# Kernel optimization log

Hardware: AMD Instinct MI355X
Metric: run time of the kernel (lower is better)

The kernel has to match this reference:

```python
import jax, jax.numpy as jnp
import numpy as np
from jax import lax

B, L, D = 2, 2048, 128
H, HD = 8, 32
WIN = 3

def setup_inputs() -> dict:
    key = jax.random.key(0)
    ks = jax.random.split(key, 7)
    s = 0.05
    return {
        "x":  jax.random.normal(ks[0], (B, L, D), jnp.float32),
        "pe": jax.random.normal(ks[1], (L, D), jnp.float32) * s,
        "Wq": jax.random.normal(ks[2], (D, H * HD), jnp.float32) * s,
        "bq": jnp.zeros((H * HD,), jnp.float32),
        "Wk": jax.random.normal(ks[3], (D, H * HD), jnp.float32) * s,
        "bk": jnp.zeros((H * HD,), jnp.float32),
        "Wv": jax.random.normal(ks[4], (D, H), jnp.float32) * s,
    }

def reference(x, pe, Wq, bq, Wk, bk, Wv):
    b, l, d = x.shape
    h = Wv.shape[1]
    hd = Wq.shape[1] // h
    xp = x + pe                                   # (B,L,D)
    # split heads: Dense output columns [i*hd:(i+1)*hd] -> head i
    q = (xp @ Wq + bq).reshape(b, l, h, hd).transpose(2, 0, 1, 3)  # (H,B,L,hd)
    k = (xp @ Wk + bk).reshape(b, l, h, hd).transpose(2, 0, 1, 3)  # (H,B,L,hd)
    v = jax.nn.sigmoid(x @ Wv).transpose(2, 0, 1)                  # (H,B,L)

    attn = jnp.einsum('hbqd,hbkd->hbqk', q, k) * (float(hd) ** -0.5)
    attn = jax.nn.softmax(attn, axis=-1)          # (H,B,L,L)

    # band_part(0,-1) + diag_part(k=(0,L-1)) (RIGHT_LEFT align) + transpose + reverse(-2,-1)
    # collapses to the skew-gather: R[p, m] = attn[L-1-p-m, L-1-p] for p+m <= L-1 else 0
    p = jnp.arange(l)[:, None]                    # (L,1)
    m = jnp.arange(l)[None, :]                    # (1,L)
    ii = l - 1 - p - m                            # row index  (L,L)
    jj = jnp.broadcast_to(l - 1 - p, (l, l))      # col index  (L,L)
    valid = (ii >= 0)
    R = attn[:, :, jnp.where(valid, ii, 0), jj] * valid.astype(attn.dtype)  # (H,B,L,L)

    R = R * v[:, :, :, None]                      # gate by value, broadcast over distance axis

    # TF avg_pool excludes padding from the divisor
    sums = lax.reduce_window(R, 0.0, lax.add, (1, 1, 1, WIN), (1, 1, 1, 1), 'SAME')
    cnt = lax.reduce_window(jnp.ones((l,), R.dtype), 0.0, lax.add, (WIN,), (1,), 'SAME')
    pooled = sums / cnt                           # (H,B,L,L)

    # global mode: sum over position axis, -> (B, L_dist, H)
    out = pooled.sum(axis=2).transpose(1, 2, 0)
    return out
```

## Files before the change

kernel.cpp:

```cpp
#include <hip/hip_runtime.h>
#include <hip/hip_bf16.h>

#define LSEQ 2048
#define BB 2
#define DD 128
#define HH 8
#define HD 32

#define FPSCALE 524288.0f
#define RFPSCALE (1.0f / 524288.0f)
#define DENSCALE 65536.0f
#define QSCALE 0.25503486f

typedef __bf16 bf8_t __attribute__((ext_vector_type(8)));
typedef __bf16 bf4_t __attribute__((ext_vector_type(4)));
typedef float f4_t __attribute__((ext_vector_type(4)));

__global__ __launch_bounds__(256) void k_A(const float* __restrict__ x,
                                           const float* __restrict__ pe,
                                           const float* __restrict__ Wq,
                                           const float* __restrict__ Wk,
                                           const float* __restrict__ Wv,
                                           const float* __restrict__ bq,
                                           const float* __restrict__ bk,
                                           float* __restrict__ w,
                                           __bf16* __restrict__ Qb,
                                           __bf16* __restrict__ Kb,
                                           int* __restrict__ Si,
                                           int* __restrict__ denI) {
    __shared__ __align__(16) char smem[34816];
    int gb = blockIdx.x;
    int tid = threadIdx.x;

    if (gb < 512) {
        __bf16* xs = (__bf16*)smem;
        __bf16* Wt = (__bf16*)(smem + 64 * 136 * 2);
        int jr = gb >> 3, y = gb & 7;
        int row0 = jr * 64;
        bool isK = y >= 4;
        int cbase = (y & 3) * 64;
        const float* W = isK ? Wk : Wq;

        #pragma unroll
        for (int i = 0; i < 8; i++) {
            int idx4 = tid + i * 256;
            int row = idx4 >> 5, col4 = idx4 & 31;
            float4 xv = ((const float4*)x)[row0 * 32 + idx4];
            float4 pv = ((const float4*)pe)[((row0 + row) & (LSEQ - 1)) * 32 + col4];
            bf4_t o = {(__bf16)(xv.x + pv.x), (__bf16)(xv.y + pv.y),
                       (__bf16)(xv.z + pv.z), (__bf16)(xv.w + pv.w)};
            *(bf4_t*)&xs[row * 136 + col4 * 4] = o;
        }
        #pragma unroll
        for (int i = 0; i < 8; i++) {
            int idx4 = tid + i * 256;
            int d = idx4 >> 4, c4 = (idx4 & 15) * 4;
            float4 wv4 = *(const float4*)(W + d * 256 + cbase + c4);
            Wt[(c4 + 0) * 136 + d] = (__bf16)wv4.x;
            Wt[(c4 + 1) * 136 + d] = (__bf16)wv4.y;
            Wt[(c4 + 2) * 136 + d] = (__bf16)wv4.z;
            Wt[(c4 + 3) * 136 + d] = (__bf16)wv4.w;
        }
        __syncthreads();

        int wid = tid >> 6, lane = tid & 63;
        int lm = lane & 15, lq = lane >> 4;
        int c0loc = wid * 16;
        f4_t acc0 = {0,0,0,0}, acc1 = {0,0,0,0}, acc2 = {0,0,0,0}, acc3 = {0,0,0,0};
        #pragma unroll
        for (int s = 0; s < 4; s++) {
            bf8_t bw = *(const bf8_t*)&Wt[(c0loc + lm) * 136 + lq * 8 + s * 32];
            bf8_t a0 = *(const bf8_t*)&xs[(0  + lm) * 136 + lq * 8 + s * 32];
            bf8_t a1 = *(const bf8_t*)&xs[(16 + lm) * 136 + lq * 8 + s * 32];
            bf8_t a2 = *(const bf8_t*)&xs[(32 + lm) * 136 + lq * 8 + s * 32];
            bf8_t a3 = *(const bf8_t*)&xs[(48 + lm) * 136 + lq * 8 + s * 32];
            acc0 = __builtin_amdgcn_mfma_f32_16x16x32_bf16(a0, bw, acc0, 0, 0, 0);
            acc1 = __builtin_amdgcn_mfma_f32_16x16x32_bf16(a1, bw, acc1, 0, 0, 0);
            acc2 = __builtin_amdgcn_mfma_f32_16x16x32_bf16(a2, bw, acc2, 0, 0, 0);
            acc3 = __builtin_amdgcn_mfma_f32_16x16x32_bf16(a3, bw, acc3, 0, 0, 0);
        }
        int c = cbase + c0loc + lm;
        float bv = (isK ? bk : bq)[c];
        float qs = isK ? 1.f : QSCALE;
        __bf16* Out = isK ? Kb : Qb;
        int h = c >> 5, hd = c & 31;
        f4_t accs[4] = {acc0, acc1, acc2, acc3};
        #pragma unroll
        for (int rs = 0; rs < 4; rs++) {
            #pragma unroll
            for (int r = 0; r < 4; r++) {
                int row = row0 + rs * 16 + lq * 4 + r;
                int b_ = row >> 11, l = row & (LSEQ - 1);
                Out[((h * BB + b_) * LSEQ + l) * HD + hd] =
                    (__bf16)((accs[rs][r] + bv) * qs);
            }
        }
    } else if (gb < 640) {
        float* xsf = (float*)smem;
        float* wvf = (float*)(smem + 32 * 132 * 4);
        int r0 = (gb - 512) * 32;
        for (int i = 0; i < 16; i++) {
            int idx = tid + i * 256;
            xsf[(idx >> 7) * 132 + (idx & 127)] = x[r0 * 128 + idx];
        }
        for (int i = 0; i < 4; i++) {
            int idx = tid + i * 256;
            wvf[idx] = Wv[idx];
        }
        __syncthreads();
        int rl = tid >> 3, h = tid & 7;
        float acc = 0.f;
        #pragma unroll 8
        for (int d = 0; d < 128; d++) acc += xsf[rl * 132 + d] * wvf[d * 8 + h];
        float sg = 1.f / (1.f + __expf(-acc));
        int r = r0 + rl;
        int b = r >> 11, l = r & (LSEQ - 1);
        w[(h * BB + b) * LSEQ + (LSEQ - 1 - l)] = sg;
    } else if (gb < 672) {
        int4 z = {0, 0, 0, 0};
        ((int4*)Si)[(gb - 640) * 256 + tid] = z;
    } else {
        int4 z = {0, 0, 0, 0};
        ((int4*)denI)[(gb - 672) * 256 + tid] = z;
    }
}

__global__ __launch_bounds__(256) void k_den(const __bf16* __restrict__ Qb,
                                             const __bf16* __restrict__ Kb,
                                             int* __restrict__ denI) {
    int hb = blockIdx.z;
    int q0 = blockIdx.y * 64;
    int kbase = blockIdx.x * 512;
    int wid = threadIdx.x >> 6, lane = threadIdx.x & 63;
    int lm = lane & 15, lq = lane >> 4;
    int qw0 = q0 + wid * 16;

    bf8_t aq = *(const bf8_t*)(Qb + (hb * LSEQ + qw0 + lm) * HD + lq * 8);
    const __bf16* Khb = Kb + hb * LSEQ * HD;

    float dsum[4] = {0.f, 0.f, 0.f, 0.f};
    #pragma unroll 4
    for (int s = 0; s < 32; s++) {
        bf8_t bk_ = *(const bf8_t*)(Khb + (kbase + s * 16 + lm) * HD + lq * 8);
        f4_t z = {0.f, 0.f, 0.f, 0.f};
        f4_t sc = __builtin_amdgcn_mfma_f32_16x16x32_bf16(aq, bk_, z, 0, 0, 0);
        #pragma unroll
        for (int r = 0; r < 4; r++) dsum[r] += exp2f(sc[r]);
    }
    #pragma unroll
    for (int r = 0; r < 4; r++) {
        float v = dsum[r];
        v += __shfl_xor(v, 1);
        v += __shfl_xor(v, 2);
        v += __shfl_xor(v, 4);
        v += __shfl_xor(v, 8);
        dsum[r] = v;
    }
    if (lm == 0) {
        #pragma unroll
        for (int r = 0; r < 4; r++)
            atomicAdd(&denI[hb * LSEQ + qw0 + lq * 4 + r],
                      __float2int_rn(dsum[r] * DENSCALE));
    }
}

__global__ __launch_bounds__(256) void k_scat(const __bf16* __restrict__ Qb,
                                              const __bf16* __restrict__ Kb,
                                              const float* __restrict__ w,
                                              const int* __restrict__ denI,
                                              int* __restrict__ S) {
    int hb = blockIdx.z;
    int q0 = blockIdx.y * 64;
    int kc0 = blockIdx.x * 256;
    if (kc0 + 256 <= q0) return;

    __shared__ int Sloc[4 * 320];
    __shared__ float wt[256];
    int tid = threadIdx.x;
    for (int i = tid; i < 1280; i += 256) Sloc[i] = 0;
    wt[tid] = w[hb * LSEQ + kc0 + tid] * FPSCALE;

    int wid = tid >> 6, lane = tid & 63;
    int lm = lane & 15, lq = lane >> 4;
    int qw0 = q0 + wid * 16;
    bf8_t aq = *(const bf8_t*)(Qb + (hb * LSEQ + qw0 + lm) * HD + lq * 8);
    float rdv[4];
    #pragma unroll
    for (int r = 0; r < 4; r++)
        rdv[r] = DENSCALE / (float)denI[hb * LSEQ + qw0 + lq * 4 + r];
    __syncthreads();

    const __bf16* Khb = Kb + hb * LSEQ * HD;
    int mbase = kc0 - q0 - 63;
    int qrow = qw0 + lq * 4;
    int* mySloc = Sloc + wid * 320;

    int sub_start = (qw0 > kc0) ? ((qw0 - kc0) >> 4) : 0;

    {
        int k0s = kc0 + sub_start * 16;
        bf8_t bk_ = *(const bf8_t*)(Khb + (k0s + lm) * HD + lq * 8);
        f4_t z = {0.f, 0.f, 0.f, 0.f};
        f4_t sc = __builtin_amdgcn_mfma_f32_16x16x32_bf16(aq, bk_, z, 0, 0, 0);
        float wvs = wt[sub_start * 16 + lm];
        int kcol = k0s + lm;
        #pragma unroll
        for (int r = 0; r < 4; r++) {
            int m = kcol - (qrow + r);
            if (m >= 0) {
                int iv = __float2int_rn(exp2f(sc[r]) * rdv[r] * wvs);
                atomicAdd(&mySloc[m - mbase], iv);
            }
        }
    }
    #pragma unroll 4
    for (int sub = sub_start + 1; sub < 16; sub++) {
        int k0s = kc0 + sub * 16;
        bf8_t bk_ = *(const bf8_t*)(Khb + (k0s + lm) * HD + lq * 8);
        f4_t z = {0.f, 0.f, 0.f, 0.f};
        f4_t sc = __builtin_amdgcn_mfma_f32_16x16x32_bf16(aq, bk_, z, 0, 0, 0);
        float wvs = wt[sub * 16 + lm];
        int kcol = k0s + lm;
        #pragma unroll
        for (int r = 0; r < 4; r++) {
            int m = kcol - (qrow + r);
            int iv = __float2int_rn(exp2f(sc[r]) * rdv[r] * wvs);
            atomicAdd(&mySloc[m - mbase], iv);
        }
    }
    __syncthreads();
    for (int i = tid; i < 320; i += 256) {
        int m = mbase + i;
        int v = Sloc[i] + Sloc[320 + i] + Sloc[640 + i] + Sloc[960 + i];
        if (m >= 0 && m < LSEQ && v != 0)
            atomicAdd(&S[hb * LSEQ + m], v);
    }
}

__global__ __launch_bounds__(256) void k_out(const int* __restrict__ S,
                                             float* __restrict__ out) {
    int idx = blockIdx.x * 256 + threadIdx.x;
    int h = idx & 7;
    int m = (idx >> 3) & (LSEQ - 1);
    int b = idx >> 14;
    const int* Sr = S + (h * BB + b) * LSEQ;
    float s = (float)Sr[m];
    float cnt = 3.f;
    if (m > 0) s += (float)Sr[m - 1]; else cnt = 2.f;
    if (m < LSEQ - 1) s += (float)Sr[m + 1]; else cnt = 2.f;
    out[idx] = s * RFPSCALE / cnt;
}

extern "C" void kernel_launch(void* const* d_in, const int* in_sizes, int n_in,
                              void* d_out, int out_size, void* d_ws, size_t ws_size,
                              hipStream_t stream) {
    const float* x  = (const float*)d_in[0];
    const float* pe = (const float*)d_in[1];
    const float* Wq = (const float*)d_in[2];
    const float* bq = (const float*)d_in[3];
    const float* Wk = (const float*)d_in[4];
    const float* bk = (const float*)d_in[5];
    const float* Wv = (const float*)d_in[6];
    float* out = (float*)d_out;

    char* ws = (char*)d_ws;
    int*    Si   = (int*)(ws);
    float*  w    = (float*)(ws + 131072);
    __bf16* Qb   = (__bf16*)(ws + 262144);
    __bf16* Kb   = (__bf16*)(ws + 262144 + 2097152);
    int*    denI = (int*)(ws + 262144 + 4194304);

    k_A<<<704, 256, 0, stream>>>(x, pe, Wq, Wk, Wv, bq, bk, w, Qb, Kb, Si, denI);
    k_den<<<dim3(4, 32, 16), 256, 0, stream>>>(Qb, Kb, denI);
    k_scat<<<dim3(8, 32, 16), 256, 0, stream>>>(Qb, Kb, w, denI, Si);
    k_out<<<128, 256, 0, stream>>>(Si, out);
}
```

Before: 128.3 us.

## Fuse denominator, scatter and output stages into one kernel with last-block finalize

Replaces the separate denominator, scatter and output kernels with a single kernel. Each block owns 16 query rows of one head-batch, computes the softmax denominator locally over all keys, then scatters gated probabilities into a shared per-distance accumulator and flushes it to global memory with atomics. The last block for each head-batch, found through an atomic counter, applies the pooling and writes the output. This removes two launches and the global denominator atomics, and also switches to the hardware exp2 and pre-scales the gate. In exchange, every block recomputes QK over all 2048 keys for its denominator, and blocks carry uneven triangular workloads.

```diff
diff --git a/kernel.cpp b/kernel.cpp
--- a/kernel.cpp
+++ b/kernel.cpp
@@ -9,12 +9,21 @@
 
 #define FPSCALE 524288.0f
 #define RFPSCALE (1.0f / 524288.0f)
-#define DENSCALE 65536.0f
 #define QSCALE 0.25503486f
 
 typedef __bf16 bf8_t __attribute__((ext_vector_type(8)));
 typedef __bf16 bf4_t __attribute__((ext_vector_type(4)));
 typedef float f4_t __attribute__((ext_vector_type(4)));
+
+static __device__ __forceinline__ float fexp2(float x) {
+#if __has_builtin(__builtin_amdgcn_exp2f)
+    return __builtin_amdgcn_exp2f(x);
+#else
+    float r;
+    asm("v_exp_f32 %0, %1" : "=v"(r) : "v"(x));
+    return r;
+#endif
+}
 
 __global__ __launch_bounds__(256) void k_A(const float* __restrict__ x,
                                            const float* __restrict__ pe,
@@ -27,7 +36,7 @@
                                            __bf16* __restrict__ Qb,
                                            __bf16* __restrict__ Kb,
                                            int* __restrict__ Si,
-                                           int* __restrict__ denI) {
+                                           int* __restrict__ cnt) {
     __shared__ __align__(16) char smem[34816];
     int gb = blockIdx.x;
     int tid = threadIdx.x;
@@ -115,37 +124,48 @@
         float sg = 1.f / (1.f + __expf(-acc));
         int r = r0 + rl;
         int b = r >> 11, l = r & (LSEQ - 1);
-        w[(h * BB + b) * LSEQ + (LSEQ - 1 - l)] = sg;
+        w[(h * BB + b) * LSEQ + (LSEQ - 1 - l)] = sg * FPSCALE;
     } else if (gb < 672) {
         int4 z = {0, 0, 0, 0};
         ((int4*)Si)[(gb - 640) * 256 + tid] = z;
     } else {
-        int4 z = {0, 0, 0, 0};
-        ((int4*)denI)[(gb - 672) * 256 + tid] = z;
-    }
-}
-
-__global__ __launch_bounds__(256) void k_den(const __bf16* __restrict__ Qb,
-                                             const __bf16* __restrict__ Kb,
-                                             int* __restrict__ denI) {
-    int hb = blockIdx.z;
-    int q0 = blockIdx.y * 64;
-    int kbase = blockIdx.x * 512;
-    int wid = threadIdx.x >> 6, lane = threadIdx.x & 63;
+        if (tid < 16) cnt[tid] = 0;
+    }
+}
+
+__global__ __launch_bounds__(256, 4) void k_F(const __bf16* __restrict__ Qb,
+                                              const __bf16* __restrict__ Kb,
+                                              const float* __restrict__ w,
+                                              int* __restrict__ S,
+                                              int* __restrict__ cnt,
+                                              float* __restrict__ out) {
+    __shared__ int Sloc[2048];
+    __shared__ float dred[64];
+    __shared__ float rdv_s[16];
+    __shared__ int lastFlag;
+
+    int hb = blockIdx.y;
+    int q0 = blockIdx.x << 4;
+    int tid = threadIdx.x;
+    int wid = tid >> 6, lane = tid & 63;
     int lm = lane & 15, lq = lane >> 4;
-    int qw0 = q0 + wid * 16;
-
-    bf8_t aq = *(const bf8_t*)(Qb + (hb * LSEQ + qw0 + lm) * HD + lq * 8);
+
+    int4 z4 = {0, 0, 0, 0};
+    ((int4*)Sloc)[tid] = z4;
+    ((int4*)Sloc)[tid + 256] = z4;
+
+    const __bf16* Qhb = Qb + hb * LSEQ * HD;
     const __bf16* Khb = Kb + hb * LSEQ * HD;
+    bf8_t aq = *(const bf8_t*)(Qhb + (q0 + lm) * HD + lq * 8);
 
     float dsum[4] = {0.f, 0.f, 0.f, 0.f};
     #pragma unroll 4
-    for (int s = 0; s < 32; s++) {
-        bf8_t bk_ = *(const bf8_t*)(Khb + (kbase + s * 16 + lm) * HD + lq * 8);
+    for (int s = wid; s < 128; s += 4) {
+        bf8_t bk_ = *(const bf8_t*)(Khb + (s * 16 + lm) * HD + lq * 8);
         f4_t z = {0.f, 0.f, 0.f, 0.f};
         f4_t sc = __builtin_amdgcn_mfma_f32_16x16x32_bf16(aq, bk_, z, 0, 0, 0);
         #pragma unroll
-        for (int r = 0; r < 4; r++) dsum[r] += exp2f(sc[r]);
+        for (int r = 0; r < 4; r++) dsum[r] += fexp2(sc[r]);
     }
     #pragma unroll
     for (int r = 0; r < 4; r++) {
@@ -158,97 +178,80 @@
     }
     if (lm == 0) {
         #pragma unroll
-        for (int r = 0; r < 4; r++)
-            atomicAdd(&denI[hb * LSEQ + qw0 + lq * 4 + r],
-                      __float2int_rn(dsum[r] * DENSCALE));
-    }
-}
-
-__global__ __launch_bounds__(256) void k_scat(const __bf16* __restrict__ Qb,
-                                              const __bf16* __restrict__ Kb,
-                                              const float* __restrict__ w,
-                                              const int* __restrict__ denI,
-                                              int* __restrict__ S) {
-    int hb = blockIdx.z;
-    int q0 = blockIdx.y * 64;
-    int kc0 = blockIdx.x * 256;
-    if (kc0 + 256 <= q0) return;
-
-    __shared__ int Sloc[4 * 320];
-    __shared__ float wt[256];
-    int tid = threadIdx.x;
-    for (int i = tid; i < 1280; i += 256) Sloc[i] = 0;
-    wt[tid] = w[hb * LSEQ + kc0 + tid] * FPSCALE;
-
-    int wid = tid >> 6, lane = tid & 63;
-    int lm = lane & 15, lq = lane >> 4;
-    int qw0 = q0 + wid * 16;
-    bf8_t aq = *(const bf8_t*)(Qb + (hb * LSEQ + qw0 + lm) * HD + lq * 8);
+        for (int r = 0; r < 4; r++) dred[wid * 16 + lq * 4 + r] = dsum[r];
+    }
+    __syncthreads();
+    if (tid < 16) {
+        float d = dred[tid] + dred[16 + tid] + dred[32 + tid] + dred[48 + tid];
+        rdv_s[tid] = 1.0f / d;
+    }
+    __syncthreads();
     float rdv[4];
     #pragma unroll
-    for (int r = 0; r < 4; r++)
-        rdv[r] = DENSCALE / (float)denI[hb * LSEQ + qw0 + lq * 4 + r];
-    __syncthreads();
-
-    const __bf16* Khb = Kb + hb * LSEQ * HD;
-    int mbase = kc0 - q0 - 63;
-    int qrow = qw0 + lq * 4;
-    int* mySloc = Sloc + wid * 320;
-
-    int sub_start = (qw0 > kc0) ? ((qw0 - kc0) >> 4) : 0;
-
-    {
-        int k0s = kc0 + sub_start * 16;
+    for (int r = 0; r < 4; r++) rdv[r] = rdv_s[lq * 4 + r];
+
+    int nsub = 128 - (q0 >> 4);
+    const float* whb = w + hb * LSEQ;
+    int qrow = q0 + lq * 4;
+    int qc = (nsub + 3) >> 2;
+    int jlo = wid * qc;
+    int jhi = jlo + qc; if (jhi > nsub) jhi = nsub;
+
+    if (wid == 0) {
+        bf8_t bk_ = *(const bf8_t*)(Khb + (q0 + lm) * HD + lq * 8);
+        f4_t z = {0.f, 0.f, 0.f, 0.f};
+        f4_t sc = __builtin_amdgcn_mfma_f32_16x16x32_bf16(aq, bk_, z, 0, 0, 0);
+        float wv = whb[q0 + lm];
+        #pragma unroll
+        for (int r = 0; r < 4; r++) {
+            int m = lm - lq * 4 - r;
+            if (m >= 0) {
+                int iv = __float2int_rn(fexp2(sc[r]) * rdv[r] * wv);
+                atomicAdd(&Sloc[m], iv);
+            }
+        }
+        jlo = 1;
+    }
+    #pragma unroll 2
+    for (int j = jlo; j < jhi; j++) {
+        int k0s = q0 + j * 16;
         bf8_t bk_ = *(const bf8_t*)(Khb + (k0s + lm) * HD + lq * 8);
         f4_t z = {0.f, 0.f, 0.f, 0.f};
         f4_t sc = __builtin_amdgcn_mfma_f32_16x16x32_bf16(aq, bk_, z, 0, 0, 0);
-        float wvs = wt[sub_start * 16 + lm];
-        int kcol = k0s + lm;
+        float wv = whb[k0s + lm];
+        int base = k0s + lm - qrow;
         #pragma unroll
         for (int r = 0; r < 4; r++) {
-            int m = kcol - (qrow + r);
-            if (m >= 0) {
-                int iv = __float2int_rn(exp2f(sc[r]) * rdv[r] * wvs);
-                atomicAdd(&mySloc[m - mbase], iv);
-            }
-        }
-    }
-    #pragma unroll 4
-    for (int sub = sub_start + 1; sub < 16; sub++) {
-        int k0s = kc0 + sub * 16;
-        bf8_t bk_ = *(const bf8_t*)(Khb + (k0s + lm) * HD + lq * 8);
-        f4_t z = {0.f, 0.f, 0.f, 0.f};
-        f4_t sc = __builtin_amdgcn_mfma_f32_16x16x32_bf16(aq, bk_, z, 0, 0, 0);
-        float wvs = wt[sub * 16 + lm];
-        int kcol = k0s + lm;
-        #pragma unroll
-        for (int r = 0; r < 4; r++) {
-            int m = kcol - (qrow + r);
-            int iv = __float2int_rn(exp2f(sc[r]) * rdv[r] * wvs);
-            atomicAdd(&mySloc[m - mbase], iv);
-        }
-    }
-    __syncthreads();
-    for (int i = tid; i < 320; i += 256) {
-        int m = mbase + i;
-        int v = Sloc[i] + Sloc[320 + i] + Sloc[640 + i] + Sloc[960 + i];
-        if (m >= 0 && m < LSEQ && v != 0)
-            atomicAdd(&S[hb * LSEQ + m], v);
-    }
-}
-
-__global__ __launch_bounds__(256) void k_out(const int* __restrict__ S,
-                                             float* __restrict__ out) {
-    int idx = blockIdx.x * 256 + threadIdx.x;
-    int h = idx & 7;
-    int m = (idx >> 3) & (LSEQ - 1);
-    int b = idx >> 14;
-    const int* Sr = S + (h * BB + b) * LSEQ;
-    float s = (float)Sr[m];
-    float cnt = 3.f;
-    if (m > 0) s += (float)Sr[m - 1]; else cnt = 2.f;
-    if (m < LSEQ - 1) s += (float)Sr[m + 1]; else cnt = 2.f;
-    out[idx] = s * RFPSCALE / cnt;
+            int iv = __float2int_rn(fexp2(sc[r]) * rdv[r] * wv);
+            atomicAdd(&Sloc[base - r], iv);
+        }
+    }
+    __syncthreads();
+
+    int M = LSEQ - q0;
+    int* Sg = S + hb * LSEQ;
+    for (int i = tid; i < M; i += 256) {
+        int v = Sloc[i];
+        if (v) atomicAdd(&Sg[i], v);
+    }
+    __threadfence();
+    __syncthreads();
+    if (tid == 0) lastFlag = (atomicAdd(&cnt[hb], 1) == 127);
+    __syncthreads();
+    if (!lastFlag) return;
+
+    for (int m = tid; m < LSEQ; m += 256)
+        Sloc[m] = __hip_atomic_load(&Sg[m], __ATOMIC_RELAXED,
+                                    __HIP_MEMORY_SCOPE_AGENT);
+    __syncthreads();
+    int h = hb >> 1, b = hb & 1;
+    for (int m = tid; m < LSEQ; m += 256) {
+        float s = (float)Sloc[m];
+        float c = 3.f;
+        if (m > 0) s += (float)Sloc[m - 1]; else c = 2.f;
+        if (m < LSEQ - 1) s += (float)Sloc[m + 1]; else c = 2.f;
+        out[(b * LSEQ + m) * 8 + h] = s * RFPSCALE / c;
+    }
 }
 
 extern "C" void kernel_launch(void* const* d_in, const int* in_sizes, int n_in,
@@ -264,14 +267,12 @@
     float* out = (float*)d_out;
 
     char* ws = (char*)d_ws;
-    int*    Si   = (int*)(ws);
-    float*  w    = (float*)(ws + 131072);
-    __bf16* Qb   = (__bf16*)(ws + 262144);
-    __bf16* Kb   = (__bf16*)(ws + 262144 + 2097152);
-    int*    denI = (int*)(ws + 262144 + 4194304);
-
-    k_A<<<704, 256, 0, stream>>>(x, pe, Wq, Wk, Wv, bq, bk, w, Qb, Kb, Si, denI);
-    k_den<<<dim3(4, 32, 16), 256, 0, stream>>>(Qb, Kb, denI);
-    k_scat<<<dim3(8, 32, 16), 256, 0, stream>>>(Qb, Kb, w, denI, Si);
-    k_out<<<128, 256, 0, stream>>>(Si, out);
-}
+    int*    Si  = (int*)(ws);
+    float*  w   = (float*)(ws + 131072);
+    __bf16* Qb  = (__bf16*)(ws + 262144);
+    __bf16* Kb  = (__bf16*)(ws + 262144 + 2097152);
+    int*    cnt = (int*)(ws + 262144 + 4194304);
+
+    k_A<<<673, 256, 0, stream>>>(x, pe, Wq, Wk, Wv, bq, bk, w, Qb, Kb, Si, cnt);
+    k_F<<<dim3(128, 16), 256, 0, stream>>>(Qb, Kb, w, Si, cnt, out);
+}
```

Result: slower. 228.5 us (+78.1%).
